# Optimization experiments

Measured on AMD Instinct MI355X. Metric: run time of the kernel, lower is better.

The kernel has to match this reference:

```python
import jax, jax.numpy as jnp
import numpy as np

# Module config (from init_kwargs): causal=False, window_size=(256,256), window_type=0,
# softmax_scale=None -> 1/sqrt(D), dropout=0 (eval mode).
WINDOW_LEFT, WINDOW_RIGHT = 256, 256


def _window_mask(Sq, Sk, causal, use_window_mask):
    """Boolean [Sq, Sk] visibility mask, FA2 semantics (right-aligned offset)."""
    qi = jnp.arange(Sq)[:, None]
    kj = jnp.arange(Sk)[None, :]
    offset = Sk - Sq
    if causal:
        return kj <= qi + offset  # window (-1, 0)
    if use_window_mask:
        m = jnp.ones((Sq, Sk), dtype=bool)
        if WINDOW_LEFT >= 0:
            m = m & (kj >= qi + offset - WINDOW_LEFT)
        if WINDOW_RIGHT >= 0:
            m = m & (kj <= qi + offset + WINDOW_RIGHT)
        return m
    return None  # full attention


def setup_inputs() -> dict:
    key = jax.random.key(0)
    kq, kkv = jax.random.split(key)
    B, Sq, Sk, H, D = 2, 2048, 2048, 16, 64
    q = jax.random.normal(kq, (B, Sq, H, D), dtype=jnp.float32)
    kv = jax.random.normal(kkv, (B, Sk, 2, H, D), dtype=jnp.float32)
    return {"q": q, "kv": kv, "causal": 0, "use_window_mask": 1, "return_attn_probs": 0}


def reference(q, kv, causal, use_window_mask, return_attn_probs):
    # q: (B, Sq, H, D); kv: (B, Sk, 2, H, D)
    B, Sq, H, D = q.shape
    Sk = kv.shape[1]
    k = kv[:, :, 0]  # (B, Sk, H, D)
    v = kv[:, :, 1]
    scale = 1.0 / (D ** 0.5)
    scores = jnp.einsum('bqhd,bkhd->bhqk', q, k) * scale  # (B, H, Sq, Sk)
    mask = _window_mask(Sq, Sk, bool(causal), bool(use_window_mask))
    if mask is not None:
        scores = jnp.where(mask[None, None], scores, jnp.finfo(scores.dtype).min)
    probs = jax.nn.softmax(scores, axis=-1)
    out = jnp.einsum('bhqk,bkhd->bqhd', probs, v)  # (B, Sq, H, D)
    return out
```

## Files before the change

kernel.cpp:

```cpp
#include <hip/hip_runtime.h>
#include <hip/hip_bf16.h>

#define B_    2
#define SQ_   2048
#define SK_   2048
#define NH_   16
#define DH_   64
#define WIN_  256
#define NEG_  -30000.0f

typedef __bf16 bf16_t;
typedef bf16_t bf16x8 __attribute__((ext_vector_type(8)));
typedef bf16_t bf16x4 __attribute__((ext_vector_type(4)));
typedef float  f32x4  __attribute__((ext_vector_type(4)));
typedef short  s16x4  __attribute__((ext_vector_type(4)));

#define KSTRIDE 72
#define VSTRIDE 72

__global__ __launch_bounds__(256, 4)
void fa_fwd(const float* __restrict__ qg, const float* __restrict__ kvg,
            float* __restrict__ outg) {
  const int tid  = threadIdx.x;
  const int wid  = tid >> 6;
  const int lane = tid & 63;
  const int quad = lane >> 4;
  const int li   = lane & 15;

  const int bid = blockIdx.x;
  const int qb  = bid >> 5;
  const int bh  = bid & 31;
  const int b   = bh >> 4;
  const int h   = bh & 15;

  const int q0b = qb * 64;
  const int q0  = q0b + wid * 16;

  __shared__ __align__(16) bf16_t sK [2][64 * KSTRIDE];
  __shared__ __align__(16) bf16_t sVT[2][64 * VSTRIDE];

  const float qscale = 0.125f * 1.44269504088896340736f;
  const float* qrow = qg + ((size_t)((b * SQ_ + q0 + li) * NH_ + h)) * DH_;
  bf16x8 qfrag[2];
#pragma unroll
  for (int c = 0; c < 2; ++c) {
    f32x4 a0 = *(const f32x4*)(qrow + c * 32 + quad * 8);
    f32x4 a1 = *(const f32x4*)(qrow + c * 32 + quad * 8 + 4);
#pragma unroll
    for (int i = 0; i < 4; ++i) {
      qfrag[c][i]     = (bf16_t)(a0[i] * qscale);
      qfrag[c][i + 4] = (bf16_t)(a1[i] * qscale);
    }
  }

  f32x4 oacc[4];
#pragma unroll
  for (int t = 0; t < 4; ++t) { f32x4 z = {0.f, 0.f, 0.f, 0.f}; oacc[t] = z; }
  float m = NEG_, l = 0.f;

  int klo = q0b - WIN_; if (klo < 0) klo = 0;
  int khi = q0b + 63 + WIN_ + 1; if (khi > SK_) khi = SK_;

  const float* kbase = kvg + (size_t)b * SK_ * 2 * NH_ * DH_ + (size_t)h * DH_;
  const float* vbase = kbase + NH_ * DH_;
  const size_t krow_stride = 2 * NH_ * DH_;

  const int skey = tid >> 2;
  const int sd0  = (tid & 3) * 16;

  f32x4 ka[4], va[4];
  {
    const float* kr = kbase + (size_t)(klo + skey) * krow_stride + sd0;
    const float* vr = vbase + (size_t)(klo + skey) * krow_stride + sd0;
#pragma unroll
    for (int i = 0; i < 4; ++i) {
      ka[i] = *(const f32x4*)(kr + 4 * i);
      va[i] = *(const f32x4*)(vr + 4 * i);
    }
  }
  {
#pragma unroll
    for (int hh = 0; hh < 2; ++hh) {
      bf16x8 wk;
#pragma unroll
      for (int i = 0; i < 4; ++i) {
        wk[i] = (bf16_t)ka[2 * hh][i]; wk[i + 4] = (bf16_t)ka[2 * hh + 1][i];
      }
      *(bf16x8*)(&sK[0][skey * KSTRIDE + sd0 + 8 * hh]) = wk;
      const int dbase = sd0 + 8 * hh;
      const int vcol  = skey ^ (((dbase >> 3) & 7) << 3);
#pragma unroll
      for (int i = 0; i < 4; ++i) {
        sVT[0][(dbase + i)     * VSTRIDE + vcol] = (bf16_t)va[2 * hh][i];
        sVT[0][(dbase + 4 + i) * VSTRIDE + vcol] = (bf16_t)va[2 * hh + 1][i];
      }
    }
  }
  __syncthreads();

  int buf = 0;
  for (int kk = klo; kk < khi; kk += 64) {
    const bool nxt = (kk + 64 < khi);
    if (nxt) {
      const float* kr = kbase + (size_t)(kk + 64 + skey) * krow_stride + sd0;
      const float* vr = vbase + (size_t)(kk + 64 + skey) * krow_stride + sd0;
#pragma unroll
      for (int i = 0; i < 4; ++i) {
        ka[i] = *(const f32x4*)(kr + 4 * i);
        va[i] = *(const f32x4*)(vr + 4 * i);
      }
    }

    if (kk + 63 >= q0 - WIN_ && kk <= q0 + 15 + WIN_) {
      f32x4 sc[4];
#pragma unroll
      for (int s = 0; s < 4; ++s) {
        bf16x8 kf0 = *(const bf16x8*)(&sK[buf][(s * 16 + li) * KSTRIDE + quad * 8]);
        bf16x8 kf1 = *(const bf16x8*)(&sK[buf][(s * 16 + li) * KSTRIDE + 32 + quad * 8]);
        f32x4 acc = {0.f, 0.f, 0.f, 0.f};
        acc = __builtin_amdgcn_mfma_f32_16x16x32_bf16(kf0, qfrag[0], acc, 0, 0, 0);
        acc = __builtin_amdgcn_mfma_f32_16x16x32_bf16(kf1, qfrag[1], acc, 0, 0, 0);
        sc[s] = acc;
      }
      if (kk < q0 - 241 || kk > q0 + 193) {
        const int qa = q0 + li;
#pragma unroll
        for (int s = 0; s < 4; ++s)
#pragma unroll
          for (int r = 0; r < 4; ++r) {
            int key = kk + s * 16 + quad * 4 + r;
            unsigned dd = (unsigned)(key - qa + WIN_);
            if (dd > 2u * WIN_) sc[s][r] = NEG_;
          }
      }
      float tl = NEG_;
#pragma unroll
      for (int s = 0; s < 4; ++s)
        tl = fmaxf(tl, fmaxf(fmaxf(sc[s][0], sc[s][1]), fmaxf(sc[s][2], sc[s][3])));

      const bool defer = (__all(tl <= m + 8.0f) != 0);
      float mnew = m;
      if (!defer) {
        float tr = fmaxf(tl, __shfl_xor(tl, 16));
        tr = fmaxf(tr, __shfl_xor(tr, 32));
        mnew = fmaxf(m, tr);
      }

      float psum = 0.f;
      bf16x4 pa[4];
#pragma unroll
      for (int s = 0; s < 4; ++s) {
        float p0 = exp2f(sc[s][0] - mnew);
        float p1 = exp2f(sc[s][1] - mnew);
        float p2 = exp2f(sc[s][2] - mnew);
        float p3 = exp2f(sc[s][3] - mnew);
        psum += (p0 + p1) + (p2 + p3);
        pa[s][0] = (bf16_t)p0; pa[s][1] = (bf16_t)p1;
        pa[s][2] = (bf16_t)p2; pa[s][3] = (bf16_t)p3;
      }

      if (!defer) {
        const float alpha = exp2f(m - mnew);
        float al[4];
#pragma unroll
        for (int r = 0; r < 4; ++r) al[r] = __shfl(alpha, quad * 4 + r);
#pragma unroll
        for (int t = 0; t < 4; ++t) {
          oacc[t][0] *= al[0]; oacc[t][1] *= al[1];
          oacc[t][2] *= al[2]; oacc[t][3] *= al[3];
        }
        l = l * alpha + psum;
        m = mnew;
      } else {
        l += psum;
      }

#pragma unroll
      for (int s = 0; s < 4; ++s) {
        const s16x4 pas = __builtin_bit_cast(s16x4, pa[s]);
#pragma unroll
        for (int t = 0; t < 4; ++t) {
          const int d  = 16 * t + li;
          const int c8 = ((2 * t + (li >> 3)) & 7) << 3;
          s16x4 vb = *(const s16x4*)(&sVT[buf][d * VSTRIDE + ((s * 16 + quad * 4) ^ c8)]);
          oacc[t] = __builtin_amdgcn_mfma_f32_16x16x16bf16_1k(pas, vb, oacc[t], 0, 0, 0);
        }
      }
    }

    if (nxt) {
#pragma unroll
      for (int hh = 0; hh < 2; ++hh) {
        bf16x8 wk;
#pragma unroll
        for (int i = 0; i < 4; ++i) {
          wk[i] = (bf16_t)ka[2 * hh][i]; wk[i + 4] = (bf16_t)ka[2 * hh + 1][i];
        }
        *(bf16x8*)(&sK[buf ^ 1][skey * KSTRIDE + sd0 + 8 * hh]) = wk;
        const int dbase = sd0 + 8 * hh;
        const int vcol  = skey ^ (((dbase >> 3) & 7) << 3);
#pragma unroll
        for (int i = 0; i < 4; ++i) {
          sVT[buf ^ 1][(dbase + i)     * VSTRIDE + vcol] = (bf16_t)va[2 * hh][i];
          sVT[buf ^ 1][(dbase + 4 + i) * VSTRIDE + vcol] = (bf16_t)va[2 * hh + 1][i];
        }
      }
    }
    __syncthreads();
    buf ^= 1;
  }

  l += __shfl_xor(l, 16);
  l += __shfl_xor(l, 32);
  float rl[4];
#pragma unroll
  for (int r = 0; r < 4; ++r) {
    float lv = __shfl(l, quad * 4 + r);
    rl[r] = 1.0f / lv;
  }
  float* orow = outg + ((size_t)((b * SQ_ + q0) * NH_ + h)) * DH_;
#pragma unroll
  for (int t = 0; t < 4; ++t)
#pragma unroll
    for (int r = 0; r < 4; ++r)
      orow[(size_t)(quad * 4 + r) * (NH_ * DH_) + 16 * t + li] = oacc[t][r] * rl[r];
}

extern "C" void kernel_launch(void* const* d_in, const int* in_sizes, int n_in,
                              void* d_out, int out_size, void* d_ws, size_t ws_size,
                              hipStream_t stream) {
  (void)in_sizes; (void)n_in; (void)out_size; (void)d_ws; (void)ws_size;
  const float* q  = (const float*)d_in[0];
  const float* kv = (const float*)d_in[1];
  float* out = (float*)d_out;
  dim3 grid(B_ * NH_ * (SQ_ / 64));
  fa_fwd<<<grid, 256, 0, stream>>>(q, kv, out);
}
```

Measured before the change: 117.9 us.

## Deepen K/V prefetch to two tiles ahead and raise MFMA wave priority

The K/V global-to-register prefetch now runs two tiles ahead. The LDS staging of the next tile moves to the start of each iteration, before compute, rather than after it, so global load latency has a full iteration of compute to hide behind. The two MFMA sections are also wrapped in s_setprio(1)/s_setprio(0) so waves issuing matrix ops get scheduling priority. The schedule must stay correct with double-buffered LDS: the next buffer is written while the current one is being read. Priority changes may not help and could disturb other waves' progress.

```diff
diff --git a/kernel.cpp b/kernel.cpp
--- a/kernel.cpp
+++ b/kernel.cpp
@@ -60,6 +60,7 @@
 
   int klo = q0b - WIN_; if (klo < 0) klo = 0;
   int khi = q0b + 63 + WIN_ + 1; if (khi > SK_) khi = SK_;
+  const int nt = (khi - klo + 63) >> 6;
 
   const float* kbase = kvg + (size_t)b * SK_ * 2 * NH_ * DH_ + (size_t)h * DH_;
   const float* vbase = kbase + NH_ * DH_;
@@ -69,16 +70,18 @@
   const int sd0  = (tid & 3) * 16;
 
   f32x4 ka[4], va[4];
-  {
-    const float* kr = kbase + (size_t)(klo + skey) * krow_stride + sd0;
-    const float* vr = vbase + (size_t)(klo + skey) * krow_stride + sd0;
+
+  auto issue_loads = [&](int kt) {
+    const float* kr = kbase + (size_t)(kt + skey) * krow_stride + sd0;
+    const float* vr = vbase + (size_t)(kt + skey) * krow_stride + sd0;
 #pragma unroll
     for (int i = 0; i < 4; ++i) {
       ka[i] = *(const f32x4*)(kr + 4 * i);
       va[i] = *(const f32x4*)(vr + 4 * i);
     }
-  }
-  {
+  };
+
+  auto stage = [&](int bb) {
 #pragma unroll
     for (int hh = 0; hh < 2; ++hh) {
       bf16x8 wk;
@@ -86,33 +89,31 @@
       for (int i = 0; i < 4; ++i) {
         wk[i] = (bf16_t)ka[2 * hh][i]; wk[i + 4] = (bf16_t)ka[2 * hh + 1][i];
       }
-      *(bf16x8*)(&sK[0][skey * KSTRIDE + sd0 + 8 * hh]) = wk;
+      *(bf16x8*)(&sK[bb][skey * KSTRIDE + sd0 + 8 * hh]) = wk;
       const int dbase = sd0 + 8 * hh;
       const int vcol  = skey ^ (((dbase >> 3) & 7) << 3);
 #pragma unroll
       for (int i = 0; i < 4; ++i) {
-        sVT[0][(dbase + i)     * VSTRIDE + vcol] = (bf16_t)va[2 * hh][i];
-        sVT[0][(dbase + 4 + i) * VSTRIDE + vcol] = (bf16_t)va[2 * hh + 1][i];
-      }
-    }
-  }
+        sVT[bb][(dbase + i)     * VSTRIDE + vcol] = (bf16_t)va[2 * hh][i];
+        sVT[bb][(dbase + 4 + i) * VSTRIDE + vcol] = (bf16_t)va[2 * hh + 1][i];
+      }
+    }
+  };
+
+  issue_loads(klo);
+  stage(0);
+  if (nt > 1) issue_loads(klo + 64);
   __syncthreads();
 
   int buf = 0;
-  for (int kk = klo; kk < khi; kk += 64) {
-    const bool nxt = (kk + 64 < khi);
-    if (nxt) {
-      const float* kr = kbase + (size_t)(kk + 64 + skey) * krow_stride + sd0;
-      const float* vr = vbase + (size_t)(kk + 64 + skey) * krow_stride + sd0;
-#pragma unroll
-      for (int i = 0; i < 4; ++i) {
-        ka[i] = *(const f32x4*)(kr + 4 * i);
-        va[i] = *(const f32x4*)(vr + 4 * i);
-      }
-    }
+  for (int t = 0; t < nt; ++t) {
+    const int kk = klo + t * 64;
+    if (t + 1 < nt) stage(buf ^ 1);
+    if (t + 2 < nt) issue_loads(klo + (t + 2) * 64);
 
     if (kk + 63 >= q0 - WIN_ && kk <= q0 + 15 + WIN_) {
       f32x4 sc[4];
+      __builtin_amdgcn_s_setprio(1);
 #pragma unroll
       for (int s = 0; s < 4; ++s) {
         bf16x8 kf0 = *(const bf16x8*)(&sK[buf][(s * 16 + li) * KSTRIDE + quad * 8]);
@@ -122,6 +123,7 @@
         acc = __builtin_amdgcn_mfma_f32_16x16x32_bf16(kf1, qfrag[1], acc, 0, 0, 0);
         sc[s] = acc;
       }
+      __builtin_amdgcn_s_setprio(0);
       if (kk < q0 - 241 || kk > q0 + 193) {
         const int qa = q0 + li;
 #pragma unroll
@@ -165,9 +167,9 @@
 #pragma unroll
         for (int r = 0; r < 4; ++r) al[r] = __shfl(alpha, quad * 4 + r);
 #pragma unroll
-        for (int t = 0; t < 4; ++t) {
-          oacc[t][0] *= al[0]; oacc[t][1] *= al[1];
-          oacc[t][2] *= al[2]; oacc[t][3] *= al[3];
+        for (int t2 = 0; t2 < 4; ++t2) {
+          oacc[t2][0] *= al[0]; oacc[t2][1] *= al[1];
+          oacc[t2][2] *= al[2]; oacc[t2][3] *= al[3];
         }
         l = l * alpha + psum;
         m = mnew;
@@ -175,37 +177,21 @@
         l += psum;
       }
 
+      __builtin_amdgcn_s_setprio(1);
 #pragma unroll
       for (int s = 0; s < 4; ++s) {
         const s16x4 pas = __builtin_bit_cast(s16x4, pa[s]);
 #pragma unroll
-        for (int t = 0; t < 4; ++t) {
-          const int d  = 16 * t + li;
-          const int c8 = ((2 * t + (li >> 3)) & 7) << 3;
+        for (int t2 = 0; t2 < 4; ++t2) {
+          const int d  = 16 * t2 + li;
+          const int c8 = ((2 * t2 + (li >> 3)) & 7) << 3;
           s16x4 vb = *(const s16x4*)(&sVT[buf][d * VSTRIDE + ((s * 16 + quad * 4) ^ c8)]);
-          oacc[t] = __builtin_amdgcn_mfma_f32_16x16x16bf16_1k(pas, vb, oacc[t], 0, 0, 0);
+          oacc[t2] = __builtin_amdgcn_mfma_f32_16x16x16bf16_1k(pas, vb, oacc[t2], 0, 0, 0);
         }
       }
-    }
-
-    if (nxt) {
-#pragma unroll
-      for (int hh = 0; hh < 2; ++hh) {
-        bf16x8 wk;
-#pragma unroll
-        for (int i = 0; i < 4; ++i) {
-          wk[i] = (bf16_t)ka[2 * hh][i]; wk[i + 4] = (bf16_t)ka[2 * hh + 1][i];
-        }
-        *(bf16x8*)(&sK[buf ^ 1][skey * KSTRIDE + sd0 + 8 * hh]) = wk;
-        const int dbase = sd0 + 8 * hh;
-        const int vcol  = skey ^ (((dbase >> 3) & 7) << 3);
-#pragma unroll
-        for (int i = 0; i < 4; ++i) {
-          sVT[buf ^ 1][(dbase + i)     * VSTRIDE + vcol] = (bf16_t)va[2 * hh][i];
-          sVT[buf ^ 1][(dbase + 4 + i) * VSTRIDE + vcol] = (bf16_t)va[2 * hh + 1][i];
-        }
-      }
-    }
+      __builtin_amdgcn_s_setprio(0);
+    }
+
     __syncthreads();
     buf ^= 1;
   }
```

After: 117.7 us. About the same (-0.1%).
